# Optimization experiments

Measured on AMD Instinct MI355X. Metric: run time of the kernel, lower is better.

The kernel has to match this reference:

```python
import jax, jax.numpy as jnp
import numpy as np

B = 8          # batch samples (decomposition_permutations)
M = 100000     # points per sample
V = 100000     # coarse voxels for max-pool/unpool (stride scaler groups)


def setup_inputs() -> dict:
    key = jax.random.key(0)
    ks = jax.random.split(key, 6)
    N = B * M
    C_in, C = 128, 128
    fea = jax.random.normal(ks[0], (N, C_in), jnp.float32)
    W1 = jax.random.normal(ks[1], (C_in, C), jnp.float32) / np.sqrt(C_in).astype(np.float32)
    b1 = jnp.zeros((C,), jnp.float32)
    W2 = jax.random.normal(ks[2], (C, 1), jnp.float32) / np.sqrt(C).astype(np.float32)
    b2 = jnp.zeros((1,), jnp.float32)
    voxel_ids = jax.random.randint(ks[3], (N,), 0, V, jnp.int32)
    target_idx = jax.random.randint(ks[4], (N // 2,), 0, N, jnp.int32)
    return dict(fea=fea, W1=W1, b1=b1, W2=W2, b2=b2,
                voxel_ids=voxel_ids, target_idx=target_idx, target_num=M // 2)


def _get_keep(p, voxel_ids, target_num):
    # MinkowskiMaxPooling + PoolingTranspose diff: per-voxel max broadcast back
    local_max = jax.ops.segment_max(p, voxel_ids, num_segments=V)[voxel_ids]
    local_max_mask = p != local_max  # points NOT equal to their local max
    pm = p.reshape(B, M)
    mm = local_max_mask.reshape(B, M)
    # kthvalue over masked values per sample: k = M - target_num (1-indexed)
    vals = jnp.where(mm, pm, jnp.inf)          # non-masked pushed to the end
    k = M - target_num
    thr = jnp.sort(vals, axis=1)[:, k - 1]     # [B] per-sample thresholds
    keep = pm > thr[:, None]                   # BCE branch: keep pred > threshold
    keep = keep | ~mm                          # keep.logical_or_(~local_max_mask)
    return keep.reshape(B * M)


def reference(fea, W1, b1, W2, b2, voxel_ids, target_idx, target_num):
    # upsample_block -> classify_block
    h = jax.nn.relu(fea @ W1 + b1)             # [N, C]
    pred = h @ W2 + b2                         # [N, 1]
    p = pred[:, 0]
    keep = _get_keep(p, voxel_ids, target_num)
    # get_target: kernel_map scatter -> keep_target (training: keep |= keep_target)
    keep_target = jnp.zeros((p.shape[0],), bool).at[target_idx].set(True)
    keep = keep | keep_target
    # MinkowskiPruning (mask instead of compaction to keep shapes static)
    out = h * keep[:, None].astype(h.dtype)
    return out, pred, keep_target
```

## Files before the change

### kernel.cpp

```cpp
#include <hip/hip_runtime.h>
#include <stdint.h>

#define BATCH 8
#define C 128
#define TPB 256
#define GEMM_BLOCKS 1024
#define TILE_R 128
#define KC 8
#define NCHUNK (C / KC)
#define HGRID 2048

__device__ __forceinline__ unsigned f2key(float f){
  unsigned b = __float_as_uint(f);
  return (b & 0x80000000u) ? ~b : (b | 0x80000000u);
}

__global__ __launch_bounds__(TPB, 1) void k_gemm(
    const float* __restrict__ fea, const float* __restrict__ W1,
    const float* __restrict__ b1, const float* __restrict__ W2,
    const float* __restrict__ b2, const int* __restrict__ vox,
    float* __restrict__ out, float* __restrict__ pred,
    unsigned* __restrict__ segkey, int N)
{
  __shared__ float sA[2][KC][TILE_R];

  const int tid  = threadIdx.x;
  const int lane = tid & 63;
  const int wid  = tid >> 6;
  const int wr   = wid >> 1;
  const int wc   = wid & 1;
  const int rowoff = wr * 64 + (lane >> 3) * 8;
  const int coloff = wc * 64 + (lane & 7) * 8;

  float b1v[8];
  #pragma unroll
  for (int i = 0; i < 8; ++i) b1v[i] = b1[coloff + i];
  const double b2d = (double)b2[0];

  const int nTiles = N / TILE_R;
  const int srow = tid >> 1;
  const int skq  = tid & 1;

  for (int tile = blockIdx.x; tile < nTiles; tile += GEMM_BLOCKS) {
    const size_t trow = (size_t)tile * TILE_R;

    float4 st = *(const float4*)(fea + (trow + srow) * C + skq * 4);
    {
      float* d = &sA[0][skq * 4][srow];
      d[0] = st.x; d[TILE_R] = st.y; d[2 * TILE_R] = st.z; d[3 * TILE_R] = st.w;
    }
    __syncthreads();

    float acc[8][8];
    #pragma unroll
    for (int j = 0; j < 8; ++j)
      #pragma unroll
      for (int i = 0; i < 8; ++i) acc[j][i] = b1v[i];

    #pragma unroll 1
    for (int kb = 0; kb < NCHUNK; ++kb) {
      if (kb + 1 < NCHUNK)
        st = *(const float4*)(fea + (trow + srow) * C + (kb + 1) * KC + skq * 4);

      const float* sAc = &sA[kb & 1][0][0];
      const float* wrow = W1 + kb * KC * C;

      float4 a0 = *(const float4*)(sAc + rowoff);
      float4 a1 = *(const float4*)(sAc + rowoff + 4);
      float4 bA = *(const float4*)(wrow + coloff);
      float4 bB = *(const float4*)(wrow + coloff + 4);

      #pragma unroll
      for (int k = 0; k < KC; ++k) {
        float4 na0, na1, nbA, nbB;
        if (k + 1 < KC) {
          na0 = *(const float4*)(sAc + (k + 1) * TILE_R + rowoff);
          na1 = *(const float4*)(sAc + (k + 1) * TILE_R + rowoff + 4);
          nbA = *(const float4*)(wrow + (k + 1) * C + coloff);
          nbB = *(const float4*)(wrow + (k + 1) * C + coloff + 4);
        }
        float af[8] = {a0.x, a0.y, a0.z, a0.w, a1.x, a1.y, a1.z, a1.w};
        float bf[8] = {bA.x, bA.y, bA.z, bA.w, bB.x, bB.y, bB.z, bB.w};
        #pragma unroll
        for (int j = 0; j < 8; ++j)
          #pragma unroll
          for (int i = 0; i < 8; ++i)
            acc[j][i] = fmaf(af[j], bf[i], acc[j][i]);
        if (k + 1 < KC) { a0 = na0; a1 = na1; bA = nbA; bB = nbB; }
      }

      if (kb + 1 < NCHUNK) {
        float* d = &sA[(kb + 1) & 1][skq * 4][srow];
        d[0] = st.x; d[TILE_R] = st.y; d[2 * TILE_R] = st.z; d[3 * TILE_R] = st.w;
      }
      __syncthreads();
    }

    float w2f[8];
    #pragma unroll
    for (int i = 0; i < 8; ++i) w2f[i] = W2[coloff + i];
    double pdv[8];
    #pragma unroll
    for (int j = 0; j < 8; ++j) {
      float hv[8];
      #pragma unroll
      for (int i = 0; i < 8; ++i) hv[i] = fmaxf(acc[j][i], 0.f);
      const size_t row = trow + rowoff + j;
      *(float4*)(out + row * C + coloff)     = make_float4(hv[0], hv[1], hv[2], hv[3]);
      *(float4*)(out + row * C + coloff + 4) = make_float4(hv[4], hv[5], hv[6], hv[7]);
      double pd = 0.0;
      #pragma unroll
      for (int i = 0; i < 8; ++i) pd += (double)hv[i] * (double)w2f[i];
      pdv[j] = pd;
    }
    #pragma unroll
    for (int j = 0; j < 8; ++j) {
      double pd = pdv[j];
      pd += __shfl_xor(pd, 1, 64);
      pd += __shfl_xor(pd, 2, 64);
      pd += __shfl_xor(pd, 4, 64);
      pdv[j] = pd;
    }
    double* sPred = (double*)&sA[0][0][0];
    if ((lane & 7) == 0) {
      #pragma unroll
      for (int j = 0; j < 8; ++j) sPred[wc * TILE_R + rowoff + j] = pdv[j];
    }
    __syncthreads();
    if (tid < TILE_R) {
      const double s = sPred[tid] + sPred[TILE_R + tid] + b2d;
      const float pv = (float)s;
      const size_t row = trow + tid;
      pred[row] = pv;
      atomicMax(&segkey[vox[row]], f2key(pv));
    }
    __syncthreads();
  }
}

__global__ __launch_bounds__(256) void k_histA(
    const float* __restrict__ pred, const int* __restrict__ vox,
    const unsigned* __restrict__ segkey, unsigned* __restrict__ valkey,
    unsigned* __restrict__ histA, int N, int M)
{
  __shared__ unsigned lh[BATCH * 256];
  for (int b = threadIdx.x; b < BATCH * 256; b += 256) lh[b] = 0;
  __syncthreads();
  const int stride = gridDim.x * 256;
  for (int i = blockIdx.x * 256 + threadIdx.x; i < N; i += stride) {
    unsigned kk = f2key(pred[i]);
    unsigned vk = (kk == segkey[vox[i]]) ? 0xFFFFFFFFu : kk;
    valkey[i] = vk;
    atomicAdd(&lh[(i / M) * 256 + (vk >> 24)], 1u);
  }
  __syncthreads();
  for (int b = threadIdx.x; b < BATCH * 256; b += 256)
    if (lh[b]) atomicAdd(&histA[b], lh[b]);
}

__global__ __launch_bounds__(256) void k_histB(
    const unsigned* __restrict__ valkey, const unsigned* __restrict__ sel,
    unsigned* __restrict__ histB, int N, int M)
{
  __shared__ unsigned lh[BATCH * 256];
  for (int b = threadIdx.x; b < BATCH * 256; b += 256) lh[b] = 0;
  __syncthreads();
  const int stride = gridDim.x * 256;
  for (int i = blockIdx.x * 256 + threadIdx.x; i < N; i += stride) {
    unsigned vk = valkey[i];
    int row = i / M;
    if ((vk >> 24) == sel[row * 4 + 0])
      atomicAdd(&lh[row * 256 + ((vk >> 16) & 255u)], 1u);
  }
  __syncthreads();
  for (int b = threadIdx.x; b < BATCH * 256; b += 256)
    if (lh[b]) atomicAdd(&histB[b], lh[b]);
}

__global__ __launch_bounds__(256) void k_histC(
    const unsigned* __restrict__ valkey, const unsigned* __restrict__ sel,
    unsigned* __restrict__ histC, int N, int M)
{
  const int stride = gridDim.x * 256;
  for (int i = blockIdx.x * 256 + threadIdx.x; i < N; i += stride) {
    unsigned vk = valkey[i];
    int row = i / M;
    if ((vk >> 16) == sel[row * 4 + 0])
      atomicAdd(&histC[(size_t)row * 65536 + (vk & 0xFFFFu)], 1u);
  }
}

__global__ void k_scan256(const unsigned* __restrict__ hist,
                          unsigned* __restrict__ sel,
                          const int* __restrict__ tnum, int M, int pass)
{
  const int row = blockIdx.x;
  __shared__ unsigned h[256];
  h[threadIdx.x] = hist[row * 256 + threadIdx.x];
  __syncthreads();
  if (threadIdx.x == 0) {
    const unsigned k = (unsigned)(M - tnum[0]);
    unsigned cum = (pass == 0) ? 0u : sel[row * 4 + 1];
    unsigned bin = 255;
    for (int i = 0; i < 256; ++i) {
      if (cum + h[i] >= k) { bin = (unsigned)i; break; }
      cum += h[i];
    }
    if (pass == 0) { sel[row * 4 + 0] = bin; }
    else           { sel[row * 4 + 0] = (sel[row * 4 + 0] << 8) | bin; }
    sel[row * 4 + 1] = cum;
  }
}

__global__ void k_scan64k(const unsigned* __restrict__ hist,
                          unsigned* __restrict__ sel,
                          const int* __restrict__ tnum, int M)
{
  const int row = blockIdx.x;
  const int t = threadIdx.x;
  const unsigned* h = hist + (size_t)row * 65536;
  __shared__ unsigned part[256];
  const uint4* hv = (const uint4*)(h + t * 256);
  unsigned s = 0;
  for (int i = 0; i < 64; ++i) { uint4 v = hv[i]; s += v.x + v.y + v.z + v.w; }
  part[t] = s;
  __syncthreads();
  if (t == 0) {
    const unsigned k = (unsigned)(M - tnum[0]);
    unsigned cum = sel[row * 4 + 1];
    int seg = 255;
    for (int i = 0; i < 256; ++i) {
      if (cum + part[i] >= k) { seg = i; break; }
      cum += part[i];
    }
    unsigned bin = 0;
    for (int i = 0; i < 256; ++i) {
      unsigned c = h[seg * 256 + i];
      if (cum + c >= k) { bin = (unsigned)(seg * 256 + i); break; }
      cum += c;
    }
    sel[row * 4 + 2] = (sel[row * 4 + 0] << 16) | bin;
  }
}

__global__ void k_scatter(const int* __restrict__ tidx, float* __restrict__ kt, int n)
{
  int i = blockIdx.x * blockDim.x + threadIdx.x;
  if (i < n) kt[tidx[i]] = 1.0f;
}

__global__ __launch_bounds__(256) void k_final(const unsigned* __restrict__ valkey,
    const float* __restrict__ kt, const unsigned* __restrict__ sel,
    float* __restrict__ out, int N, int M)
{
  const int wid = threadIdx.x >> 6;
  const int lane = threadIdx.x & 63;
  const int nw = gridDim.x * 4;
  for (int r = blockIdx.x * 4 + wid; r < N; r += nw) {
    unsigned vk = valkey[r];
    float kv = kt[r];
    unsigned thr = sel[(r / M) * 4 + 2];
    bool keep = (vk > thr) || (kv != 0.0f);
    if (!keep)
      *(float2*)&out[(size_t)r * C + lane * 2] = make_float2(0.f, 0.f);
  }
}

extern "C" void kernel_launch(void* const* d_in, const int* in_sizes, int n_in,
                              void* d_out, int out_size, void* d_ws, size_t ws_size,
                              hipStream_t stream)
{
  const float* fea = (const float*)d_in[0];
  const float* W1  = (const float*)d_in[1];
  const float* b1  = (const float*)d_in[2];
  const float* W2  = (const float*)d_in[3];
  const float* b2  = (const float*)d_in[4];
  const int* vox   = (const int*)d_in[5];
  const int* tidx  = (const int*)d_in[6];
  const int* tnum  = (const int*)d_in[7];

  const int N = in_sizes[5];
  const int M = N / BATCH;
  const int nT = in_sizes[6];

  float* out  = (float*)d_out;
  float* pred = out + (size_t)N * C;
  float* kt   = pred + N;

  char* w = (char*)d_ws;
  unsigned* segkey = (unsigned*)(w);
  unsigned* histA  = (unsigned*)(w + (512u << 10));
  unsigned* histB  = (unsigned*)(w + (520u << 10));
  unsigned* sel    = (unsigned*)(w + (528u << 10));
  unsigned* histC  = (unsigned*)(w + (532u << 10));
  unsigned* valkey = (unsigned*)(w + (532u << 10) + (2u << 20));

  const size_t zbytes = (532u << 10) + (2u << 20);
  hipMemsetAsync(d_ws, 0, zbytes, stream);
  hipMemsetAsync(kt, 0, (size_t)N * sizeof(float), stream);

  k_scatter<<<(nT + 255) / 256, 256, 0, stream>>>(tidx, kt, nT);
  k_gemm<<<GEMM_BLOCKS, TPB, 0, stream>>>(fea, W1, b1, W2, b2, vox,
                                          out, pred, segkey, N);
  k_histA<<<HGRID, 256, 0, stream>>>(pred, vox, segkey, valkey, histA, N, M);
  k_scan256<<<BATCH, 256, 0, stream>>>(histA, sel, tnum, M, 0);
  k_histB<<<HGRID, 256, 0, stream>>>(valkey, sel, histB, N, M);
  k_scan256<<<BATCH, 256, 0, stream>>>(histB, sel, tnum, M, 1);
  k_histC<<<HGRID, 256, 0, stream>>>(valkey, sel, histC, N, M);
  k_scan64k<<<BATCH, 256, 0, stream>>>(histC, sel, tnum, M);
  k_final<<<2048, 256, 0, stream>>>(valkey, kt, sel, out, N, M);
}
```

Measured before the change: 550.8 us.

## Stage transposed W1 in swizzled LDS and stream A rows from registers

The GEMM kernel now loads all of W1 once per block into shared memory, transposed with an XOR swizzle, instead of re-reading W1 from global memory on every K-chunk. Each thread reads its own 8 rows of fea straight from global memory into registers with float4 loads, double-buffered over k-groups, so the per-chunk LDS staging and barriers are gone. The grid is halved to 512 blocks because the 64 KB of shared memory per block limits occupancy. The cost is higher register pressure and per-thread strided global reads of A, which give up the coalescing of the old cooperative tile loads.

```diff
diff --git a/kernel.cpp b/kernel.cpp
--- a/kernel.cpp
+++ b/kernel.cpp
@@ -4,10 +4,8 @@
 #define BATCH 8
 #define C 128
 #define TPB 256
-#define GEMM_BLOCKS 1024
+#define GEMM_BLOCKS 512
 #define TILE_R 128
-#define KC 8
-#define NCHUNK (C / KC)
 #define HGRID 2048
 
 __device__ __forceinline__ unsigned f2key(float f){
@@ -22,7 +20,8 @@
     float* __restrict__ out, float* __restrict__ pred,
     unsigned* __restrict__ segkey, int N)
 {
-  __shared__ float sA[2][KC][TILE_R];
+  __shared__ float sW1t[C * C];
+  __shared__ double sPredS[2 * TILE_R];
 
   const int tid  = threadIdx.x;
   const int lane = tid & 63;
@@ -31,25 +30,28 @@
   const int wc   = wid & 1;
   const int rowoff = wr * 64 + (lane >> 3) * 8;
   const int coloff = wc * 64 + (lane & 7) * 8;
-
+  const int lmask  = lane & 7;
+
+  for (int idx = tid; idx < C * C; idx += TPB) {
+    int k = idx >> 7, c = idx & 127;
+    sW1t[c * C + (((k >> 2) ^ ((c >> 3) & 7)) << 2) + (k & 3)] = W1[idx];
+  }
   float b1v[8];
   #pragma unroll
   for (int i = 0; i < 8; ++i) b1v[i] = b1[coloff + i];
   const double b2d = (double)b2[0];
+  __syncthreads();
 
   const int nTiles = N / TILE_R;
-  const int srow = tid >> 1;
-  const int skq  = tid & 1;
+  const float* bcol = &sW1t[coloff * C];
 
   for (int tile = blockIdx.x; tile < nTiles; tile += GEMM_BLOCKS) {
     const size_t trow = (size_t)tile * TILE_R;
-
-    float4 st = *(const float4*)(fea + (trow + srow) * C + skq * 4);
-    {
-      float* d = &sA[0][skq * 4][srow];
-      d[0] = st.x; d[TILE_R] = st.y; d[2 * TILE_R] = st.z; d[3 * TILE_R] = st.w;
-    }
-    __syncthreads();
+    const float* abase = fea + (trow + rowoff) * C;
+
+    float4 Aa[8], Ab[8];
+    #pragma unroll
+    for (int j = 0; j < 8; ++j) Aa[j] = *(const float4*)(abase + j * C);
 
     float acc[8][8];
     #pragma unroll
@@ -58,42 +60,51 @@
       for (int i = 0; i < 8; ++i) acc[j][i] = b1v[i];
 
     #pragma unroll 1
-    for (int kb = 0; kb < NCHUNK; ++kb) {
-      if (kb + 1 < NCHUNK)
-        st = *(const float4*)(fea + (trow + srow) * C + (kb + 1) * KC + skq * 4);
-
-      const float* sAc = &sA[kb & 1][0][0];
-      const float* wrow = W1 + kb * KC * C;
-
-      float4 a0 = *(const float4*)(sAc + rowoff);
-      float4 a1 = *(const float4*)(sAc + rowoff + 4);
-      float4 bA = *(const float4*)(wrow + coloff);
-      float4 bB = *(const float4*)(wrow + coloff + 4);
-
-      #pragma unroll
-      for (int k = 0; k < KC; ++k) {
-        float4 na0, na1, nbA, nbB;
-        if (k + 1 < KC) {
-          na0 = *(const float4*)(sAc + (k + 1) * TILE_R + rowoff);
-          na1 = *(const float4*)(sAc + (k + 1) * TILE_R + rowoff + 4);
-          nbA = *(const float4*)(wrow + (k + 1) * C + coloff);
-          nbB = *(const float4*)(wrow + (k + 1) * C + coloff + 4);
+    for (int kg = 0; kg < 32; kg += 2) {
+      #pragma unroll
+      for (int j = 0; j < 8; ++j)
+        Ab[j] = *(const float4*)(abase + j * C + (kg + 1) * 4);
+      {
+        const int goff = ((kg ^ lmask) << 2);
+        float4 Bv[8];
+        #pragma unroll
+        for (int i = 0; i < 8; ++i)
+          Bv[i] = *(const float4*)(bcol + i * C + goff);
+        #pragma unroll
+        for (int j = 0; j < 8; ++j) {
+          #pragma unroll
+          for (int i = 0; i < 8; ++i) acc[j][i] = fmaf(Aa[j].x, Bv[i].x, acc[j][i]);
+          #pragma unroll
+          for (int i = 0; i < 8; ++i) acc[j][i] = fmaf(Aa[j].y, Bv[i].y, acc[j][i]);
+          #pragma unroll
+          for (int i = 0; i < 8; ++i) acc[j][i] = fmaf(Aa[j].z, Bv[i].z, acc[j][i]);
+          #pragma unroll
+          for (int i = 0; i < 8; ++i) acc[j][i] = fmaf(Aa[j].w, Bv[i].w, acc[j][i]);
         }
-        float af[8] = {a0.x, a0.y, a0.z, a0.w, a1.x, a1.y, a1.z, a1.w};
-        float bf[8] = {bA.x, bA.y, bA.z, bA.w, bB.x, bB.y, bB.z, bB.w};
+      }
+      if (kg + 2 < 32) {
         #pragma unroll
         for (int j = 0; j < 8; ++j)
-          #pragma unroll
-          for (int i = 0; i < 8; ++i)
-            acc[j][i] = fmaf(af[j], bf[i], acc[j][i]);
-        if (k + 1 < KC) { a0 = na0; a1 = na1; bA = nbA; bB = nbB; }
+          Aa[j] = *(const float4*)(abase + j * C + (kg + 2) * 4);
       }
-
-      if (kb + 1 < NCHUNK) {
-        float* d = &sA[(kb + 1) & 1][skq * 4][srow];
-        d[0] = st.x; d[TILE_R] = st.y; d[2 * TILE_R] = st.z; d[3 * TILE_R] = st.w;
+      {
+        const int goff = (((kg + 1) ^ lmask) << 2);
+        float4 Bv[8];
+        #pragma unroll
+        for (int i = 0; i < 8; ++i)
+          Bv[i] = *(const float4*)(bcol + i * C + goff);
+        #pragma unroll
+        for (int j = 0; j < 8; ++j) {
+          #pragma unroll
+          for (int i = 0; i < 8; ++i) acc[j][i] = fmaf(Ab[j].x, Bv[i].x, acc[j][i]);
+          #pragma unroll
+          for (int i = 0; i < 8; ++i) acc[j][i] = fmaf(Ab[j].y, Bv[i].y, acc[j][i]);
+          #pragma unroll
+          for (int i = 0; i < 8; ++i) acc[j][i] = fmaf(Ab[j].z, Bv[i].z, acc[j][i]);
+          #pragma unroll
+          for (int i = 0; i < 8; ++i) acc[j][i] = fmaf(Ab[j].w, Bv[i].w, acc[j][i]);
+        }
       }
-      __syncthreads();
     }
 
     float w2f[8];
@@ -121,14 +132,13 @@
       pd += __shfl_xor(pd, 4, 64);
       pdv[j] = pd;
     }
-    double* sPred = (double*)&sA[0][0][0];
     if ((lane & 7) == 0) {
       #pragma unroll
-      for (int j = 0; j < 8; ++j) sPred[wc * TILE_R + rowoff + j] = pdv[j];
+      for (int j = 0; j < 8; ++j) sPredS[wc * TILE_R + rowoff + j] = pdv[j];
     }
     __syncthreads();
     if (tid < TILE_R) {
-      const double s = sPred[tid] + sPred[TILE_R + tid] + b2d;
+      const double s = sPredS[tid] + sPredS[TILE_R + tid] + b2d;
       const float pv = (float)s;
       const size_t row = trow + tid;
       pred[row] = pv;
```

After: 557.8 us. About the same (+1.3%).
